# Kernel tuning notes

Hardware: AMD Instinct MI355X
Metric: run time of the kernel (lower is better)

Reference implementation:

```python
import jax, jax.numpy as jnp
import numpy as np

N_NODES = 200000
N_EDGES = 400000
N_GRAPHS = 4096
IN_DIM, HID_DIM, OUT_DIM, EDGE_DIM = 128, 256, 256, 16


def setup_inputs() -> dict:
    key = jax.random.key(0)
    ks = jax.random.split(key, 16)
    x = jax.random.normal(ks[0], (N_NODES, IN_DIM), dtype=jnp.float32)
    edge_attr = jax.random.normal(ks[1], (N_EDGES, EDGE_DIM), dtype=jnp.float32)
    edge_index = jax.random.randint(ks[2], (2, N_EDGES), 0, N_NODES, dtype=jnp.int64)
    batch = jnp.sort(jax.random.randint(ks[3], (N_NODES,), 0, N_GRAPHS, dtype=jnp.int64))

    def lin(k, fan_in, fan_out):
        bound = 1.0 / np.sqrt(fan_in)
        kw, kb = jax.random.split(k)
        W = jax.random.uniform(kw, (fan_in, fan_out), minval=-bound, maxval=bound, dtype=jnp.float32)
        b = jax.random.uniform(kb, (fan_out,), minval=-bound, maxval=bound, dtype=jnp.float32)
        return W, b

    We1, be1 = lin(ks[4], EDGE_DIM, IN_DIM)    # GINEConv1 edge projection
    W1a, b1a = lin(ks[5], IN_DIM, HID_DIM)     # conv1 MLP layer 1
    W1b, b1b = lin(ks[6], HID_DIM, HID_DIM)    # conv1 MLP layer 2
    We2, be2 = lin(ks[7], EDGE_DIM, HID_DIM)   # GINEConv2 edge projection
    W2a, b2a = lin(ks[8], HID_DIM, HID_DIM)    # conv2 MLP layer 1
    W2b, b2b = lin(ks[9], HID_DIM, OUT_DIM)    # conv2 MLP layer 2
    return {"x": x, "edge_attr": edge_attr,
            "We1": We1, "be1": be1, "W1a": W1a, "b1a": b1a, "W1b": W1b, "b1b": b1b,
            "We2": We2, "be2": be2, "W2a": W2a, "b2a": b2a, "W2b": W2b, "b2b": b2b,
            "edge_index": edge_index, "batch": batch}


def _gine_conv(x, edge_attr, src, dst, We, be, Wa, ba, Wb, bb):
    # messages: relu(x_j + lin_edge(e)), scatter-add into destination nodes
    e_proj = edge_attr @ We + be                      # [E, D]
    msg = jax.nn.relu(x[src] + e_proj)                # [E, D]
    aggr = jax.ops.segment_sum(msg, dst, num_segments=x.shape[0])  # [N, D]
    h = x + aggr                                      # (1 + eps) * x_i + aggr, eps=0
    h = jax.nn.relu(h @ Wa + ba)
    return h @ Wb + bb


def reference(x, edge_attr, We1, be1, W1a, b1a, W1b, b1b,
              We2, be2, W2a, b2a, W2b, b2b, edge_index, batch):
    src, dst = edge_index[0], edge_index[1]
    h = jax.nn.relu(_gine_conv(x, edge_attr, src, dst, We1, be1, W1a, b1a, W1b, b1b))
    h = jax.nn.relu(_gine_conv(h, edge_attr, src, dst, We2, be2, W2a, b2a, W2b, b2b))
    # global mean pool over graphs
    sums = jax.ops.segment_sum(h, batch, num_segments=N_GRAPHS)            # [G, D]
    counts = jax.ops.segment_sum(jnp.ones((h.shape[0],), h.dtype), batch,
                                 num_segments=N_GRAPHS)                    # [G]
    return sums / jnp.maximum(counts, 1.0)[:, None]
```

## Files before the change

kernel.cpp:

```cpp
#include <hip/hip_runtime.h>
#include <hip/hip_bf16.h>

typedef float f32x4 __attribute__((ext_vector_type(4)));
typedef float f32x2 __attribute__((ext_vector_type(2)));
typedef unsigned short u16x2 __attribute__((ext_vector_type(2)));
typedef unsigned short u16x4 __attribute__((ext_vector_type(4)));
typedef unsigned short u16x8 __attribute__((ext_vector_type(8)));
typedef short s16x8 __attribute__((ext_vector_type(8)));

#define NN 200000
#define NE 400000
#define NG 4096
#define SCHUNK 1024
#define NSCAN ((NN + SCHUNK - 1) / SCHUNK)

template<int C> struct VecT;
template<> struct VecT<2> { using T = u16x2; };
template<> struct VecT<4> { using T = u16x4; };

__device__ __forceinline__ unsigned short f2bf(float f) {
    union { float f; unsigned int u; } v; v.f = f;
    unsigned int r = v.u + 0x7FFF + ((v.u >> 16) & 1);
    return (unsigned short)(r >> 16);
}
__device__ __forceinline__ float bf2f(unsigned short b) {
    union { unsigned int u; float f; } v; v.u = ((unsigned int)b) << 16;
    return v.f;
}

__global__ void detect_i64(const int* __restrict__ ei, int* __restrict__ flag) {
    unsigned long long m = __ballot(ei[threadIdx.x * 2 + 1] == 0);
    if (threadIdx.x == 0) *flag = (~m == 0ULL) ? 1 : 0;
}
__device__ __forceinline__ int load_idx(const int* p, long long i, int f64) {
    return f64 ? (int)((const long long*)p)[i] : p[i];
}

__global__ void wt_conv(const float* __restrict__ W, unsigned short* __restrict__ Wt,
                        int K, int N) {
    int tid = blockIdx.x * 256 + threadIdx.x;
    if (tid >= K * N) return;
    int n = tid / K, k = tid - n * K;
    Wt[tid] = f2bf(W[(size_t)k * N + n]);
}

__global__ __launch_bounds__(256) void x2bf(const float* __restrict__ x,
                                            unsigned short* __restrict__ xh) {
    long long i = ((long long)blockIdx.x * 256 + threadIdx.x) * 4;
    if (i >= (long long)NN * 128) return;
    f32x4 v = *(const f32x4*)(x + i);
    u16x4 o; o.x = f2bf(v.x); o.y = f2bf(v.y); o.z = f2bf(v.z); o.w = f2bf(v.w);
    *(u16x4*)(xh + i) = o;
}

__global__ __launch_bounds__(256) void ea_perm(const float* __restrict__ ea,
                                               const int* __restrict__ eidx,
                                               const int* __restrict__ totE_p,
                                               float* __restrict__ eac) {
    int j = blockIdx.x * 256 + threadIdx.x;
    if (j >= *totE_p) return;
    int e = eidx[j];
    if ((unsigned)e >= NE) e = 0;
    const float* s = ea + (size_t)e * 16;
    float* d = eac + (size_t)j * 16;
#pragma unroll
    for (int k = 0; k < 4; ++k)
        *(f32x4*)(d + k * 4) = *(const f32x4*)(s + k * 4);
}

__global__ __launch_bounds__(256) void hist_dst(const int* __restrict__ ei,
                                                const int* __restrict__ flag,
                                                int* __restrict__ deg) {
    int e = blockIdx.x * 256 + threadIdx.x;
    if (e >= NE) return;
    int f64 = *flag;
    int s = load_idx(ei, e, f64);
    int d = load_idx(ei, (long long)NE + e, f64);
    if ((unsigned)s < NN && (unsigned)d < NN) atomicAdd(&deg[d], 1);
}

__global__ __launch_bounds__(256) void scan_bsum(const int* __restrict__ deg,
                                                 int* __restrict__ bsum) {
    __shared__ int red[256];
    int t = threadIdx.x, base = blockIdx.x * SCHUNK + t * 4;
    int s = 0;
#pragma unroll
    for (int c = 0; c < 4; ++c) { int i = base + c; if (i < NN) s += deg[i]; }
    red[t] = s; __syncthreads();
    for (int o = 128; o > 0; o >>= 1) { if (t < o) red[t] += red[t + o]; __syncthreads(); }
    if (t == 0) bsum[blockIdx.x] = red[0];
}

__global__ void scan_carry(int* __restrict__ bsum, int* __restrict__ rowptr_end) {
    if (threadIdx.x == 0) {
        int run = 0;
        for (int i = 0; i < NSCAN; ++i) { int v = bsum[i]; bsum[i] = run; run += v; }
        *rowptr_end = run;
    }
}

__global__ __launch_bounds__(256) void scan_final(const int* __restrict__ deg,
                                                  const int* __restrict__ bsum,
                                                  int* __restrict__ rowptr,
                                                  int* __restrict__ cursor) {
    __shared__ int lds[256];
    int t = threadIdx.x, base = blockIdx.x * SCHUNK + t * 4;
    int v[4], s = 0;
#pragma unroll
    for (int c = 0; c < 4; ++c) { int i = base + c; v[c] = (i < NN) ? deg[i] : 0; s += v[c]; }
    lds[t] = s; __syncthreads();
    for (int o = 1; o < 256; o <<= 1) {
        int x = 0;
        if (t >= o) x = lds[t - o];
        __syncthreads();
        if (t >= o) lds[t] += x;
        __syncthreads();
    }
    int run = lds[t] - s + bsum[blockIdx.x];
#pragma unroll
    for (int c = 0; c < 4; ++c) {
        int i = base + c;
        if (i < NN) { rowptr[i] = run; cursor[i] = run; }
        run += v[c];
    }
}

__global__ __launch_bounds__(256) void fill_csr(const int* __restrict__ ei,
                                                const int* __restrict__ flag,
                                                int* __restrict__ cursor,
                                                int* __restrict__ srcs,
                                                int* __restrict__ eidx) {
    int e = blockIdx.x * 256 + threadIdx.x;
    if (e >= NE) return;
    int f64 = *flag;
    int s = load_idx(ei, e, f64);
    int d = load_idx(ei, (long long)NE + e, f64);
    if ((unsigned)s >= NN || (unsigned)d >= NN) return;
    int pos = atomicAdd(&cursor[d], 1);
    if ((unsigned)pos < NE) { srcs[pos] = s; eidx[pos] = e; }
}

template<int C, int U>
__global__ __launch_bounds__(256)
void msg_build(const unsigned short* __restrict__ xh,
               const float* __restrict__ eac,
               const float* __restrict__ We, const float* __restrict__ be,
               const int* __restrict__ srcs, const int* __restrict__ totE_p,
               unsigned short* __restrict__ M) {
    using XV = typename VecT<C>::T;
    constexpr int D = 64 * C;
    constexpr int C2 = C / 2;
    const int wid  = (blockIdx.x * 256 + threadIdx.x) >> 6;
    const int lane = threadIdx.x & 63;
    const int totE = *totE_p;
    const int col = lane * C;

    f32x2 w2[16][C2], bb2[C2];
#pragma unroll
    for (int k = 0; k < 16; ++k)
#pragma unroll
        for (int c = 0; c < C2; ++c)
            w2[k][c] = *(const f32x2*)(We + k * D + col + 2 * c);
#pragma unroll
    for (int c = 0; c < C2; ++c) bb2[c] = *(const f32x2*)(be + col + 2 * c);

    const int j0 = wid * U;
    int sv[U];
    XV xv[U];
#pragma unroll
    for (int u = 0; u < U; ++u) {
        int j = j0 + u;
        sv[u] = (j < totE) ? srcs[j] : -1;
    }
#pragma unroll
    for (int u = 0; u < U; ++u) {
        if ((unsigned)sv[u] < NN)
            xv[u] = *(const XV*)(xh + (size_t)sv[u] * D + col);
        else
            xv[u] = (XV)0;
    }
#pragma unroll
    for (int u = 0; u < U; ++u) {
        int j = j0 + u;
        if (j >= totE) continue;
        const float* eap = eac + (size_t)j * 16;
        f32x4 e0 = *(const f32x4*)eap;
        f32x4 e1 = *(const f32x4*)(eap + 4);
        f32x4 e2 = *(const f32x4*)(eap + 8);
        f32x4 e3 = *(const f32x4*)(eap + 12);
        f32x2 m2[C2];
#pragma unroll
        for (int c = 0; c < C2; ++c) {
            f32x2 xx; xx.x = bf2f(xv[u][2 * c]); xx.y = bf2f(xv[u][2 * c + 1]);
            m2[c] = bb2[c] + xx;
        }
#pragma unroll
        for (int k = 0; k < 4; ++k) {
            f32x2 k0; k0.x = e0[k]; k0.y = e0[k];
            f32x2 k1; k1.x = e1[k]; k1.y = e1[k];
            f32x2 k2; k2.x = e2[k]; k2.y = e2[k];
            f32x2 k3; k3.x = e3[k]; k3.y = e3[k];
#pragma unroll
            for (int c = 0; c < C2; ++c) {
                m2[c] += k0 * w2[k][c];
                m2[c] += k1 * w2[4 + k][c];
                m2[c] += k2 * w2[8 + k][c];
                m2[c] += k3 * w2[12 + k][c];
            }
        }
        XV o;
#pragma unroll
        for (int c = 0; c < C2; ++c) {
            o[2 * c]     = f2bf(fmaxf(m2[c].x, 0.f));
            o[2 * c + 1] = f2bf(fmaxf(m2[c].y, 0.f));
        }
        *(XV*)(M + (size_t)j * D + col) = o;
    }
}

template<int C>
__global__ __launch_bounds__(256)
void seg_sum(const unsigned short* __restrict__ M, const int* __restrict__ rowptr,
             const unsigned short* __restrict__ self, unsigned short* __restrict__ outp) {
    using XV = typename VecT<C>::T;
    constexpr int D = 64 * C;
    const int node = (blockIdx.x * 256 + threadIdx.x) >> 6;
    const int lane = threadIdx.x & 63;
    if (node >= NN) return;
    const int col = lane * C;
    int lo = rowptr[node], hi = rowptr[node + 1];
    if (lo > hi || (unsigned)hi > NE) { lo = 0; hi = 0; }

    float a[C];
    XV sv = *(const XV*)(self + (size_t)node * D + col);
#pragma unroll
    for (int c = 0; c < C; ++c) a[c] = bf2f(sv[c]);

    int j = lo;
    for (; j + 1 < hi; j += 2) {
        XV m0 = *(const XV*)(M + (size_t)j * D + col);
        XV m1 = *(const XV*)(M + (size_t)(j + 1) * D + col);
#pragma unroll
        for (int c = 0; c < C; ++c) a[c] += bf2f(m0[c]) + bf2f(m1[c]);
    }
    if (j < hi) {
        XV m0 = *(const XV*)(M + (size_t)j * D + col);
#pragma unroll
        for (int c = 0; c < C; ++c) a[c] += bf2f(m0[c]);
    }
    XV o;
#pragma unroll
    for (int c = 0; c < C; ++c) o[c] = f2bf(a[c]);
    *(XV*)(outp + (size_t)node * D + col) = o;
}

template<int K1, typename CT>
__global__ __launch_bounds__(256)
void gemm2_fused(const unsigned short* __restrict__ A,
                 const unsigned short* __restrict__ Wta, const float* __restrict__ ba,
                 const unsigned short* __restrict__ Wtb, const float* __restrict__ bb,
                 CT* __restrict__ C) {
    constexpr int LDT = 68;
    constexpr int LDM = 260;
    __shared__ unsigned short As[64 * LDT];
    __shared__ unsigned short Bs[256 * LDT];
    __shared__ unsigned short Ms[64 * LDM];
    const int m0 = blockIdx.x * 64;
    const int tid = threadIdx.x;
    const int wave = tid >> 6;
    const int lane = tid & 63;
    const int lm = lane & 15;
    const int lq = lane >> 4;
    const int nw = wave * 64;

    const int srow = tid >> 2;
    const int scol = (tid & 3) * 16;

    {
        f32x4 acc[4][4] = {};
        for (int k0 = 0; k0 < K1; k0 += 64) {
            {
                const unsigned short* src = A + (size_t)(m0 + srow) * K1 + k0 + scol;
                unsigned short* dst = As + srow * LDT + scol;
                *(u16x8*)(dst)     = *(const u16x8*)(src);
                *(u16x8*)(dst + 8) = *(const u16x8*)(src + 8);
            }
#pragma unroll
            for (int rr = 0; rr < 4; ++rr) {
                int r = srow + rr * 64;
                const unsigned short* src = Wta + (size_t)r * K1 + k0 + scol;
                unsigned short* dst = Bs + r * LDT + scol;
                *(u16x8*)(dst)     = *(const u16x8*)(src);
                *(u16x8*)(dst + 8) = *(const u16x8*)(src + 8);
            }
            __syncthreads();
#pragma unroll
            for (int ks = 0; ks < 2; ++ks) {
                s16x8 af[4], bf[4];
#pragma unroll
                for (int mt = 0; mt < 4; ++mt)
                    af[mt] = *(const s16x8*)(As + (mt * 16 + lm) * LDT + ks * 32 + lq * 8);
#pragma unroll
                for (int nt = 0; nt < 4; ++nt)
                    bf[nt] = *(const s16x8*)(Bs + (nw + nt * 16 + lm) * LDT + ks * 32 + lq * 8);
#pragma unroll
                for (int mt = 0; mt < 4; ++mt)
#pragma unroll
                    for (int nt = 0; nt < 4; ++nt)
                        acc[mt][nt] = __builtin_amdgcn_mfma_f32_16x16x32_bf16(
                            af[mt], bf[nt], acc[mt][nt], 0, 0, 0);
            }
            __syncthreads();
        }
#pragma unroll
        for (int mt = 0; mt < 4; ++mt) {
            const int row = mt * 16 + lq * 4;
#pragma unroll
            for (int nt = 0; nt < 4; ++nt) {
                int coln = nw + nt * 16 + lm;
                float bv = ba[coln];
#pragma unroll
                for (int r = 0; r < 4; ++r) {
                    float v = fmaxf(acc[mt][nt][r] + bv, 0.f);
                    Ms[(row + r) * LDM + coln] = f2bf(v);
                }
            }
        }
    }
    __syncthreads();

    {
        f32x4 acc[4][4] = {};
        for (int k0 = 0; k0 < 256; k0 += 64) {
#pragma unroll
            for (int rr = 0; rr < 4; ++rr) {
                int r = srow + rr * 64;
                const unsigned short* src = Wtb + (size_t)r * 256 + k0 + scol;
                unsigned short* dst = Bs + r * LDT + scol;
                *(u16x8*)(dst)     = *(const u16x8*)(src);
                *(u16x8*)(dst + 8) = *(const u16x8*)(src + 8);
            }
            __syncthreads();
#pragma unroll
            for (int ks = 0; ks < 2; ++ks) {
                s16x8 af[4], bf[4];
#pragma unroll
                for (int mt = 0; mt < 4; ++mt)
                    af[mt] = *(const s16x8*)(Ms + (mt * 16 + lm) * LDM + k0 + ks * 32 + lq * 8);
#pragma unroll
                for (int nt = 0; nt < 4; ++nt)
                    bf[nt] = *(const s16x8*)(Bs + (nw + nt * 16 + lm) * LDT + ks * 32 + lq * 8);
#pragma unroll
                for (int mt = 0; mt < 4; ++mt)
#pragma unroll
                    for (int nt = 0; nt < 4; ++nt)
                        acc[mt][nt] = __builtin_amdgcn_mfma_f32_16x16x32_bf16(
                            af[mt], bf[nt], acc[mt][nt], 0, 0, 0);
            }
            __syncthreads();
        }
#pragma unroll
        for (int mt = 0; mt < 4; ++mt) {
            const int row = m0 + mt * 16 + lq * 4;
#pragma unroll
            for (int nt = 0; nt < 4; ++nt) {
                int coln = nw + nt * 16 + lm;
                float bv = bb[coln];
#pragma unroll
                for (int r = 0; r < 4; ++r) {
                    float v = fmaxf(acc[mt][nt][r] + bv, 0.f);
                    if constexpr (sizeof(CT) == 2)
                        C[(size_t)(row + r) * 256 + coln] = (CT)f2bf(v);
                    else
                        C[(size_t)(row + r) * 256 + coln] = (CT)v;
                }
            }
        }
    }
}

__global__ __launch_bounds__(256)
void pool_mean(const float* __restrict__ h, const int* __restrict__ batch,
               const int* __restrict__ flag, float* __restrict__ out) {
    const int f64 = *flag;
    int g = blockIdx.x;
    int a = 0, b = NN;
    while (a < b) { int m = (a + b) >> 1; if (load_idx(batch, m, f64) < g) a = m + 1; else b = m; }
    int lo = a;
    b = NN;
    while (a < b) { int m = (a + b) >> 1; if (load_idx(batch, m, f64) < g + 1) a = m + 1; else b = m; }
    int hi = a;
    int f = threadIdx.x;
    float s = 0.f;
    for (int n = lo; n < hi; ++n) s += h[(size_t)n * 256 + f];
    float cnt = (float)(hi - lo);
    out[(size_t)g * 256 + f] = s / fmaxf(cnt, 1.f);
}

extern "C" void kernel_launch(void* const* d_in, const int* in_sizes, int n_in,
                              void* d_out, int out_size, void* d_ws, size_t ws_size,
                              hipStream_t stream) {
    const float* x   = (const float*)d_in[0];
    const float* ea  = (const float*)d_in[1];
    const float* We1 = (const float*)d_in[2];
    const float* be1 = (const float*)d_in[3];
    const float* W1a = (const float*)d_in[4];
    const float* b1a = (const float*)d_in[5];
    const float* W1b = (const float*)d_in[6];
    const float* b1b = (const float*)d_in[7];
    const float* We2 = (const float*)d_in[8];
    const float* be2 = (const float*)d_in[9];
    const float* W2a = (const float*)d_in[10];
    const float* b2a = (const float*)d_in[11];
    const float* W2b = (const float*)d_in[12];
    const float* b2b = (const float*)d_in[13];
    const int*   ei  = (const int*)d_in[14];
    const int*   bat = (const int*)d_in[15];
    float* out = (float*)d_out;

    char* ws = (char*)d_ws;
    const size_t SZH = (size_t)NN * 256 * 2;
    unsigned short* A  = (unsigned short*)ws;
    unsigned short* B  = (unsigned short*)(ws + SZH);
    unsigned short* Cr = (unsigned short*)(ws + 2 * SZH);
    char* Dr = ws + 3 * SZH;
    char* q = Dr;
    int* deg    = (int*)q; q += (size_t)NN * 4;
    int* rowptr = (int*)q; q += (size_t)(NN + 1) * 4;
    int* cursor = (int*)q; q += (size_t)NN * 4;
    int* srcs   = (int*)q; q += (size_t)NE * 4;
    int* eidx   = (int*)q; q += (size_t)NE * 4;
    int* bsum   = (int*)q; q += (size_t)NSCAN * 4;
    q = Dr + ((q - Dr + 63) & ~63ll);
    float*          eac = (float*)q; q += (size_t)NE * 16 * 4;
    unsigned short* xh  = (unsigned short*)q;
    char* p = ws + 4 * SZH;
    unsigned short* Wt1a = (unsigned short*)p; p += 128 * 256 * 2;
    unsigned short* Wt1b = (unsigned short*)p; p += 256 * 256 * 2;
    unsigned short* Wt2a = (unsigned short*)p; p += 256 * 256 * 2;
    unsigned short* Wt2b = (unsigned short*)p; p += 256 * 256 * 2;
    int* flag = (int*)p;

    detect_i64<<<1, 64, 0, stream>>>(ei, flag);
    wt_conv<<<(128 * 256 + 255) / 256, 256, 0, stream>>>(W1a, Wt1a, 128, 256);
    wt_conv<<<(256 * 256 + 255) / 256, 256, 0, stream>>>(W1b, Wt1b, 256, 256);
    wt_conv<<<(256 * 256 + 255) / 256, 256, 0, stream>>>(W2a, Wt2a, 256, 256);
    wt_conv<<<(256 * 256 + 255) / 256, 256, 0, stream>>>(W2b, Wt2b, 256, 256);

    hipMemsetAsync(deg, 0, (size_t)NN * 4, stream);
    hist_dst<<<(NE + 255) / 256, 256, 0, stream>>>(ei, flag, deg);
    scan_bsum<<<NSCAN, 256, 0, stream>>>(deg, bsum);
    scan_carry<<<1, 64, 0, stream>>>(bsum, rowptr + NN);
    scan_final<<<NSCAN, 256, 0, stream>>>(deg, bsum, rowptr, cursor);
    fill_csr<<<(NE + 255) / 256, 256, 0, stream>>>(ei, flag, cursor, srcs, eidx);
    ea_perm<<<(NE + 255) / 256, 256, 0, stream>>>(ea, eidx, rowptr + NN, eac);
    x2bf<<<(NN * 128 / 4 + 255) / 256, 256, 0, stream>>>(x, xh);

    const int GM_BLK = NE / 32;
    const int GS_BLK = NN / 4;
    const int GG_BLK = NN / 64;

    msg_build<2, 8><<<GM_BLK, 256, 0, stream>>>(xh, eac, We1, be1, srcs, rowptr + NN, A);
    seg_sum<2><<<GS_BLK, 256, 0, stream>>>(A, rowptr, xh, B);
    gemm2_fused<128, unsigned short><<<GG_BLK, 256, 0, stream>>>(B, Wt1a, b1a, Wt1b, b1b, A);

    msg_build<4, 8><<<GM_BLK, 256, 0, stream>>>(A, eac, We2, be2, srcs, rowptr + NN, B);
    seg_sum<4><<<GS_BLK, 256, 0, stream>>>(B, rowptr, A, A);
    gemm2_fused<256, float><<<GG_BLK, 256, 0, stream>>>(A, Wt2a, b2a, Wt2b, b2b, (float*)Cr);

    pool_mean<<<NG, 256, 0, stream>>>((const float*)Cr, bat, flag, out);
}
```

Baseline: 934.2 us.

## Fuse global mean-pool sums into second GEMM epilogue with atomics, shrink K tile

The final fused MLP GEMM no longer writes a 200k x 256 fp32 activation buffer. Its epilogue now reduces each tile's rows per graph using the sorted batch ids and atomically adds the partial sums into a small per-graph buffer. A light kernel then divides by the node counts. The GEMM K-step also drops from 64 to 32 and the A tile shares LDS with the intermediate, which cuts LDS use and may raise occupancy, at the cost of more barriers per K. It also adds a batch-index conversion kernel, a memset, and float atomics whose summation order is nondeterministic.

```diff
diff --git a/kernel.cpp b/kernel.cpp
--- a/kernel.cpp
+++ b/kernel.cpp
@@ -34,6 +34,13 @@
 }
 __device__ __forceinline__ int load_idx(const int* p, long long i, int f64) {
     return f64 ? (int)((const long long*)p)[i] : p[i];
+}
+
+__global__ __launch_bounds__(256) void bat_conv(const int* __restrict__ bat,
+                                                const int* __restrict__ flag,
+                                                int* __restrict__ bat32) {
+    int i = blockIdx.x * 256 + threadIdx.x;
+    if (i < NN) bat32[i] = *flag ? (int)((const long long*)bat)[i] : bat[i];
 }
 
 __global__ void wt_conv(const float* __restrict__ W, unsigned short* __restrict__ Wt,
@@ -254,17 +261,17 @@
     *(XV*)(outp + (size_t)node * D + col) = o;
 }
 
-template<int K1, typename CT>
+template<int K1, int MODE>
 __global__ __launch_bounds__(256)
 void gemm2_fused(const unsigned short* __restrict__ A,
                  const unsigned short* __restrict__ Wta, const float* __restrict__ ba,
                  const unsigned short* __restrict__ Wtb, const float* __restrict__ bb,
-                 CT* __restrict__ C) {
-    constexpr int LDT = 68;
+                 unsigned short* __restrict__ C,
+                 float* __restrict__ sums, const int* __restrict__ bat32) {
+    constexpr int LDT = 36;
     constexpr int LDM = 260;
-    __shared__ unsigned short As[64 * LDT];
+    __shared__ unsigned short Us[64 * LDM];
     __shared__ unsigned short Bs[256 * LDT];
-    __shared__ unsigned short Ms[64 * LDM];
     const int m0 = blockIdx.x * 64;
     const int tid = threadIdx.x;
     const int wave = tid >> 6;
@@ -273,92 +280,89 @@
     const int lq = lane >> 4;
     const int nw = wave * 64;
 
-    const int srow = tid >> 2;
-    const int scol = (tid & 3) * 16;
-
-    {
-        f32x4 acc[4][4] = {};
-        for (int k0 = 0; k0 < K1; k0 += 64) {
-            {
-                const unsigned short* src = A + (size_t)(m0 + srow) * K1 + k0 + scol;
-                unsigned short* dst = As + srow * LDT + scol;
-                *(u16x8*)(dst)     = *(const u16x8*)(src);
-                *(u16x8*)(dst + 8) = *(const u16x8*)(src + 8);
+    const int arow = tid >> 2;
+    const int aseg = (tid & 3) * 8;
+    const int brow = tid >> 1;
+    const int bcol = (tid & 1) * 16;
+
+    f32x4 acc[4][4] = {};
+
+    for (int k0 = 0; k0 < K1; k0 += 32) {
+        *(u16x8*)(Us + arow * LDT + aseg) =
+            *(const u16x8*)(A + (size_t)(m0 + arow) * K1 + k0 + aseg);
+        {
+            const unsigned short* s0 = Wta + (size_t)brow * K1 + k0 + bcol;
+            const unsigned short* s1 = Wta + (size_t)(brow + 128) * K1 + k0 + bcol;
+            unsigned short* d0 = Bs + brow * LDT + bcol;
+            unsigned short* d1 = Bs + (brow + 128) * LDT + bcol;
+            *(u16x8*)(d0)     = *(const u16x8*)(s0);
+            *(u16x8*)(d0 + 8) = *(const u16x8*)(s0 + 8);
+            *(u16x8*)(d1)     = *(const u16x8*)(s1);
+            *(u16x8*)(d1 + 8) = *(const u16x8*)(s1 + 8);
+        }
+        __syncthreads();
+        s16x8 af[4], bf[4];
+#pragma unroll
+        for (int mt = 0; mt < 4; ++mt)
+            af[mt] = *(const s16x8*)(Us + (mt * 16 + lm) * LDT + lq * 8);
+#pragma unroll
+        for (int nt = 0; nt < 4; ++nt)
+            bf[nt] = *(const s16x8*)(Bs + (nw + nt * 16 + lm) * LDT + lq * 8);
+#pragma unroll
+        for (int mt = 0; mt < 4; ++mt)
+#pragma unroll
+            for (int nt = 0; nt < 4; ++nt)
+                acc[mt][nt] = __builtin_amdgcn_mfma_f32_16x16x32_bf16(
+                    af[mt], bf[nt], acc[mt][nt], 0, 0, 0);
+        __syncthreads();
+    }
+
+#pragma unroll
+    for (int mt = 0; mt < 4; ++mt) {
+        const int row = mt * 16 + lq * 4;
+#pragma unroll
+        for (int nt = 0; nt < 4; ++nt) {
+            int coln = nw + nt * 16 + lm;
+            float bv = ba[coln];
+#pragma unroll
+            for (int r = 0; r < 4; ++r) {
+                float v = fmaxf(acc[mt][nt][r] + bv, 0.f);
+                Us[(row + r) * LDM + coln] = f2bf(v);
+                acc[mt][nt][r] = 0.f;
             }
-#pragma unroll
-            for (int rr = 0; rr < 4; ++rr) {
-                int r = srow + rr * 64;
-                const unsigned short* src = Wta + (size_t)r * K1 + k0 + scol;
-                unsigned short* dst = Bs + r * LDT + scol;
-                *(u16x8*)(dst)     = *(const u16x8*)(src);
-                *(u16x8*)(dst + 8) = *(const u16x8*)(src + 8);
-            }
-            __syncthreads();
-#pragma unroll
-            for (int ks = 0; ks < 2; ++ks) {
-                s16x8 af[4], bf[4];
-#pragma unroll
-                for (int mt = 0; mt < 4; ++mt)
-                    af[mt] = *(const s16x8*)(As + (mt * 16 + lm) * LDT + ks * 32 + lq * 8);
-#pragma unroll
-                for (int nt = 0; nt < 4; ++nt)
-                    bf[nt] = *(const s16x8*)(Bs + (nw + nt * 16 + lm) * LDT + ks * 32 + lq * 8);
-#pragma unroll
-                for (int mt = 0; mt < 4; ++mt)
-#pragma unroll
-                    for (int nt = 0; nt < 4; ++nt)
-                        acc[mt][nt] = __builtin_amdgcn_mfma_f32_16x16x32_bf16(
-                            af[mt], bf[nt], acc[mt][nt], 0, 0, 0);
-            }
-            __syncthreads();
-        }
-#pragma unroll
-        for (int mt = 0; mt < 4; ++mt) {
-            const int row = mt * 16 + lq * 4;
-#pragma unroll
-            for (int nt = 0; nt < 4; ++nt) {
-                int coln = nw + nt * 16 + lm;
-                float bv = ba[coln];
-#pragma unroll
-                for (int r = 0; r < 4; ++r) {
-                    float v = fmaxf(acc[mt][nt][r] + bv, 0.f);
-                    Ms[(row + r) * LDM + coln] = f2bf(v);
-                }
-            }
         }
     }
     __syncthreads();
 
-    {
-        f32x4 acc[4][4] = {};
-        for (int k0 = 0; k0 < 256; k0 += 64) {
-#pragma unroll
-            for (int rr = 0; rr < 4; ++rr) {
-                int r = srow + rr * 64;
-                const unsigned short* src = Wtb + (size_t)r * 256 + k0 + scol;
-                unsigned short* dst = Bs + r * LDT + scol;
-                *(u16x8*)(dst)     = *(const u16x8*)(src);
-                *(u16x8*)(dst + 8) = *(const u16x8*)(src + 8);
-            }
-            __syncthreads();
-#pragma unroll
-            for (int ks = 0; ks < 2; ++ks) {
-                s16x8 af[4], bf[4];
-#pragma unroll
-                for (int mt = 0; mt < 4; ++mt)
-                    af[mt] = *(const s16x8*)(Ms + (mt * 16 + lm) * LDM + k0 + ks * 32 + lq * 8);
-#pragma unroll
-                for (int nt = 0; nt < 4; ++nt)
-                    bf[nt] = *(const s16x8*)(Bs + (nw + nt * 16 + lm) * LDT + ks * 32 + lq * 8);
-#pragma unroll
-                for (int mt = 0; mt < 4; ++mt)
-#pragma unroll
-                    for (int nt = 0; nt < 4; ++nt)
-                        acc[mt][nt] = __builtin_amdgcn_mfma_f32_16x16x32_bf16(
-                            af[mt], bf[nt], acc[mt][nt], 0, 0, 0);
-            }
-            __syncthreads();
-        }
+    for (int k0 = 0; k0 < 256; k0 += 32) {
+        {
+            const unsigned short* s0 = Wtb + (size_t)brow * 256 + k0 + bcol;
+            const unsigned short* s1 = Wtb + (size_t)(brow + 128) * 256 + k0 + bcol;
+            unsigned short* d0 = Bs + brow * LDT + bcol;
+            unsigned short* d1 = Bs + (brow + 128) * LDT + bcol;
+            *(u16x8*)(d0)     = *(const u16x8*)(s0);
+            *(u16x8*)(d0 + 8) = *(const u16x8*)(s0 + 8);
+            *(u16x8*)(d1)     = *(const u16x8*)(s1);
+            *(u16x8*)(d1 + 8) = *(const u16x8*)(s1 + 8);
+        }
+        __syncthreads();
+        s16x8 af[4], bf[4];
+#pragma unroll
+        for (int mt = 0; mt < 4; ++mt)
+            af[mt] = *(const s16x8*)(Us + (mt * 16 + lm) * LDM + k0 + lq * 8);
+#pragma unroll
+        for (int nt = 0; nt < 4; ++nt)
+            bf[nt] = *(const s16x8*)(Bs + (nw + nt * 16 + lm) * LDT + lq * 8);
+#pragma unroll
+        for (int mt = 0; mt < 4; ++mt)
+#pragma unroll
+            for (int nt = 0; nt < 4; ++nt)
+                acc[mt][nt] = __builtin_amdgcn_mfma_f32_16x16x32_bf16(
+                    af[mt], bf[nt], acc[mt][nt], 0, 0, 0);
+        __syncthreads();
+    }
+
+    if constexpr (MODE == 0) {
 #pragma unroll
         for (int mt = 0; mt < 4; ++mt) {
             const int row = m0 + mt * 16 + lq * 4;
@@ -369,32 +373,48 @@
 #pragma unroll
                 for (int r = 0; r < 4; ++r) {
                     float v = fmaxf(acc[mt][nt][r] + bv, 0.f);
-                    if constexpr (sizeof(CT) == 2)
-                        C[(size_t)(row + r) * 256 + coln] = (CT)f2bf(v);
-                    else
-                        C[(size_t)(row + r) * 256 + coln] = (CT)v;
+                    C[(size_t)(row + r) * 256 + coln] = f2bf(v);
                 }
             }
         }
+    } else {
+        int g16[16];
+#pragma unroll
+        for (int mt = 0; mt < 4; ++mt)
+#pragma unroll
+            for (int r = 0; r < 4; ++r)
+                g16[mt * 4 + r] = bat32[m0 + mt * 16 + lq * 4 + r];
+#pragma unroll
+        for (int nt = 0; nt < 4; ++nt) {
+            int coln = nw + nt * 16 + lm;
+            float bv = bb[coln];
+            int curg = g16[0];
+            float s = 0.f;
+#pragma unroll
+            for (int i = 0; i < 16; ++i) {
+                float v = fmaxf(acc[i >> 2][nt][i & 3] + bv, 0.f);
+                if (g16[i] != curg) {
+                    if ((unsigned)curg < NG) atomicAdd(&sums[(size_t)curg * 256 + coln], s);
+                    curg = g16[i]; s = 0.f;
+                }
+                s += v;
+            }
+            if ((unsigned)curg < NG) atomicAdd(&sums[(size_t)curg * 256 + coln], s);
+        }
     }
 }
 
 __global__ __launch_bounds__(256)
-void pool_mean(const float* __restrict__ h, const int* __restrict__ batch,
-               const int* __restrict__ flag, float* __restrict__ out) {
-    const int f64 = *flag;
+void pool_div(const float* __restrict__ sums, const int* __restrict__ bat32,
+              float* __restrict__ out) {
     int g = blockIdx.x;
     int a = 0, b = NN;
-    while (a < b) { int m = (a + b) >> 1; if (load_idx(batch, m, f64) < g) a = m + 1; else b = m; }
+    while (a < b) { int m = (a + b) >> 1; if (bat32[m] < g) a = m + 1; else b = m; }
     int lo = a;
     b = NN;
-    while (a < b) { int m = (a + b) >> 1; if (load_idx(batch, m, f64) < g + 1) a = m + 1; else b = m; }
-    int hi = a;
-    int f = threadIdx.x;
-    float s = 0.f;
-    for (int n = lo; n < hi; ++n) s += h[(size_t)n * 256 + f];
-    float cnt = (float)(hi - lo);
-    out[(size_t)g * 256 + f] = s / fmaxf(cnt, 1.f);
+    while (a < b) { int m = (a + b) >> 1; if (bat32[m] < g + 1) a = m + 1; else b = m; }
+    float inv = 1.f / fmaxf((float)(a - lo), 1.f);
+    out[(size_t)g * 256 + threadIdx.x] = sums[(size_t)g * 256 + threadIdx.x] * inv;
 }
 
 extern "C" void kernel_launch(void* const* d_in, const int* in_sizes, int n_in,
@@ -422,7 +442,6 @@
     const size_t SZH = (size_t)NN * 256 * 2;
     unsigned short* A  = (unsigned short*)ws;
     unsigned short* B  = (unsigned short*)(ws + SZH);
-    unsigned short* Cr = (unsigned short*)(ws + 2 * SZH);
     char* Dr = ws + 3 * SZH;
     char* q = Dr;
     int* deg    = (int*)q; q += (size_t)NN * 4;
@@ -433,7 +452,9 @@
     int* bsum   = (int*)q; q += (size_t)NSCAN * 4;
     q = Dr + ((q - Dr + 63) & ~63ll);
     float*          eac = (float*)q; q += (size_t)NE * 16 * 4;
-    unsigned short* xh  = (unsigned short*)q;
+    unsigned short* xh  = (unsigned short*)q; q += (size_t)NN * 128 * 2;
+    int*   bat32 = (int*)q;   q += (size_t)NN * 4;
+    float* sums  = (float*)q; q += (size_t)NG * 256 * 4;
     char* p = ws + 4 * SZH;
     unsigned short* Wt1a = (unsigned short*)p; p += 128 * 256 * 2;
     unsigned short* Wt1b = (unsigned short*)p; p += 256 * 256 * 2;
@@ -442,12 +463,14 @@
     int* flag = (int*)p;
 
     detect_i64<<<1, 64, 0, stream>>>(ei, flag);
+    bat_conv<<<(NN + 255) / 256, 256, 0, stream>>>(bat, flag, bat32);
     wt_conv<<<(128 * 256 + 255) / 256, 256, 0, stream>>>(W1a, Wt1a, 128, 256);
     wt_conv<<<(256 * 256 + 255) / 256, 256, 0, stream>>>(W1b, Wt1b, 256, 256);
     wt_conv<<<(256 * 256 + 255) / 256, 256, 0, stream>>>(W2a, Wt2a, 256, 256);
     wt_conv<<<(256 * 256 + 255) / 256, 256, 0, stream>>>(W2b, Wt2b, 256, 256);
 
     hipMemsetAsync(deg, 0, (size_t)NN * 4, stream);
+    hipMemsetAsync(sums, 0, (size_t)NG * 256 * 4, stream);
     hist_dst<<<(NE + 255) / 256, 256, 0, stream>>>(ei, flag, deg);
     scan_bsum<<<NSCAN, 256, 0, stream>>>(deg, bsum);
     scan_carry<<<1, 64, 0, stream>>>(bsum, rowptr + NN);
@@ -462,11 +485,13 @@
 
     msg_build<2, 8><<<GM_BLK, 256, 0, stream>>>(xh, eac, We1, be1, srcs, rowptr + NN, A);
     seg_sum<2><<<GS_BLK, 256, 0, stream>>>(A, rowptr, xh, B);
-    gemm2_fused<128, unsigned short><<<GG_BLK, 256, 0, stream>>>(B, Wt1a, b1a, Wt1b, b1b, A);
+    gemm2_fused<128, 0><<<GG_BLK, 256, 0, stream>>>(B, Wt1a, b1a, Wt1b, b1b, A,
+                                                    nullptr, nullptr);
 
     msg_build<4, 8><<<GM_BLK, 256, 0, stream>>>(A, eac, We2, be2, srcs, rowptr + NN, B);
     seg_sum<4><<<GS_BLK, 256, 0, stream>>>(B, rowptr, A, A);
-    gemm2_fused<256, float><<<GG_BLK, 256, 0, stream>>>(A, Wt2a, b2a, Wt2b, b2b, (float*)Cr);
-
-    pool_mean<<<NG, 256, 0, stream>>>((const float*)Cr, bat, flag, out);
-}
+    gemm2_fused<256, 1><<<GG_BLK, 256, 0, stream>>>(A, Wt2a, b2a, Wt2b, b2b, nullptr,
+                                                    sums, bat32);
+
+    pool_div<<<NG, 256, 0, stream>>>(sums, bat32, out);
+}
```

Result: faster. 913.7 us (-2.2%).
